# Kernel optimization log

Hardware: AMD Instinct MI355X
Metric: run time of the kernel (lower is better)

The kernel has to match this reference:

```python
import jax, jax.numpy as jnp
import numpy as np

NEG_BIG = -1e10
LEAKY_ALPHA = 0.2

def setup_inputs() -> dict:
    key = jax.random.key(0)
    k1, k2, k3, k4 = jax.random.split(key, 4)
    B, N, F, H = 8, 2048, 128, 4
    X = jax.random.normal(k1, (B, N, F), dtype=jnp.float32)
    A = jax.random.bernoulli(k2, 0.06, (B, N, N)).astype(jnp.float32)
    A = jnp.maximum(A, jnp.eye(N, dtype=jnp.float32)[None])
    attn_self = jax.random.normal(k3, (H, F), dtype=jnp.float32) * 0.1
    attn_neigh = jax.random.normal(k4, (H, F), dtype=jnp.float32) * 0.1
    return {"X": X, "A": A, "attn_self": attn_self, "attn_neigh": attn_neigh}

def reference(X, A, attn_self, attn_neigh):
    # mode 0, concat reduction, tanh activation (applied per head, as in call_mode0)
    B, N, F = X.shape
    H = attn_self.shape[0]
    a_self = jnp.einsum('bnf,hf->bhn', X, attn_self)   # [B,H,N]
    a_neigh = jnp.einsum('bnf,hf->bhn', X, attn_neigh)  # [B,H,N]
    dense = a_self[:, :, :, None] + a_neigh[:, :, None, :]  # [B,H,N,N]
    dense = jnp.where(dense >= 0, dense, LEAKY_ALPHA * dense)  # leaky relu 0.2
    mask = jnp.where(A == 0.0, NEG_BIG, 0.0)[:, None, :, :]   # [B,1,N,N]
    attn = jax.nn.softmax(dense + mask, axis=-1)               # [B,H,N,N]
    feats = jnp.einsum('bhnm,bmf->bhnf', attn, X)              # [B,H,N,F]
    feats = jnp.tanh(feats)
    # concat heads on feature axis -> [B,N,H*F]
    return feats.transpose(0, 2, 1, 3).reshape(B, N, H * F)
```

## Files before the change

### kernel.cpp

```cpp
#include <hip/hip_runtime.h>
#include <hip/hip_bf16.h>
#include <math.h>

#define N_NODES 2048
#define F_DIM   128
#define H_HEADS 4
#define B_BATCH 8
#define LEAKY   0.2f

typedef float f32x4 __attribute__((ext_vector_type(4)));
typedef float f32x2 __attribute__((ext_vector_type(2)));

__device__ __forceinline__ float tanh_fast(float x) {
    const float e = __expf(2.0f * x);
    return 1.0f - 2.0f / (e + 1.0f);
}

__global__ __launch_bounds__(256) void gat_bitpack(const float* __restrict__ A,
                                                   unsigned char* __restrict__ maskb) {
    const int row = blockIdx.x;
    const int tid = threadIdx.x;
    const f32x4* Ar = (const f32x4*)(A + (size_t)row * N_NODES);
    const f32x4 a0 = __builtin_nontemporal_load(Ar + tid * 2);
    const f32x4 a1 = __builtin_nontemporal_load(Ar + tid * 2 + 1);
    unsigned b = 0;
    b |= (a0.x != 0.0f ? 1u : 0u) << 0;
    b |= (a0.y != 0.0f ? 1u : 0u) << 1;
    b |= (a0.z != 0.0f ? 1u : 0u) << 2;
    b |= (a0.w != 0.0f ? 1u : 0u) << 3;
    b |= (a1.x != 0.0f ? 1u : 0u) << 4;
    b |= (a1.y != 0.0f ? 1u : 0u) << 5;
    b |= (a1.z != 0.0f ? 1u : 0u) << 6;
    b |= (a1.w != 0.0f ? 1u : 0u) << 7;
    maskb[(size_t)row * 256 + tid] = (unsigned char)b;
}

__global__ __launch_bounds__(256) void gat_proj(const float* __restrict__ X,
                                                const float* __restrict__ wS,
                                                const float* __restrict__ wN,
                                                float* __restrict__ aSt,
                                                float* __restrict__ aNt) {
    const int wave = threadIdx.x >> 6;
    const int lane = threadIdx.x & 63;
    const int row  = blockIdx.x * 4 + wave;
    const float* xr = X + (size_t)row * F_DIM;
    const float x0 = xr[lane];
    const float x1 = xr[lane + 64];
    float4 ps4, pn4;
    float* psv = (float*)&ps4;
    float* pnv = (float*)&pn4;
#pragma unroll
    for (int h = 0; h < H_HEADS; ++h) {
        float ps = x0 * wS[h * F_DIM + lane] + x1 * wS[h * F_DIM + 64 + lane];
        float pn = x0 * wN[h * F_DIM + lane] + x1 * wN[h * F_DIM + 64 + lane];
#pragma unroll
        for (int off = 32; off > 0; off >>= 1) {
            ps += __shfl_xor(ps, off);
            pn += __shfl_xor(pn, off);
        }
        psv[h] = ps;
        pnv[h] = pn;
    }
    if (lane == 0) {
        ((float4*)aSt)[row] = ps4;
        ((float4*)aNt)[row] = pn4;
    }
}

__global__ __launch_bounds__(256) void gat_gmax(const float* __restrict__ aNt,
                                                float* __restrict__ gmax) {
    const int b = blockIdx.x;
    const int tid = threadIdx.x;
    const int lane = tid & 63;
    const int wv = tid >> 6;
    __shared__ float4 s_part[4];
    float4 m = make_float4(-1e30f, -1e30f, -1e30f, -1e30f);
    const float4* src = (const float4*)aNt + (size_t)b * N_NODES;
    for (int n = tid; n < N_NODES; n += 256) {
        const float4 v = src[n];
        m.x = fmaxf(m.x, v.x); m.y = fmaxf(m.y, v.y);
        m.z = fmaxf(m.z, v.z); m.w = fmaxf(m.w, v.w);
    }
#pragma unroll
    for (int off = 32; off > 0; off >>= 1) {
        m.x = fmaxf(m.x, __shfl_xor(m.x, off));
        m.y = fmaxf(m.y, __shfl_xor(m.y, off));
        m.z = fmaxf(m.z, __shfl_xor(m.z, off));
        m.w = fmaxf(m.w, __shfl_xor(m.w, off));
    }
    if (lane == 0) s_part[wv] = m;
    __syncthreads();
    if (tid == 0) {
        float4 r = s_part[0];
#pragma unroll
        for (int w = 1; w < 4; ++w) {
            r.x = fmaxf(r.x, s_part[w].x); r.y = fmaxf(r.y, s_part[w].y);
            r.z = fmaxf(r.z, s_part[w].z); r.w = fmaxf(r.w, s_part[w].w);
        }
        ((float4*)gmax)[b] = r;
    }
}

#define FMA16(PV, XV)                                        \
    do {                                                     \
        acc[0][0] = fmaf((PV).x, (XV).x, acc[0][0]);         \
        acc[0][1] = fmaf((PV).x, (XV).y, acc[0][1]);         \
        acc[0][2] = fmaf((PV).x, (XV).z, acc[0][2]);         \
        acc[0][3] = fmaf((PV).x, (XV).w, acc[0][3]);         \
        acc[1][0] = fmaf((PV).y, (XV).x, acc[1][0]);         \
        acc[1][1] = fmaf((PV).y, (XV).y, acc[1][1]);         \
        acc[1][2] = fmaf((PV).y, (XV).z, acc[1][2]);         \
        acc[1][3] = fmaf((PV).y, (XV).w, acc[1][3]);         \
        acc[2][0] = fmaf((PV).z, (XV).x, acc[2][0]);         \
        acc[2][1] = fmaf((PV).z, (XV).y, acc[2][1]);         \
        acc[2][2] = fmaf((PV).z, (XV).z, acc[2][2]);         \
        acc[2][3] = fmaf((PV).z, (XV).w, acc[2][3]);         \
        acc[3][0] = fmaf((PV).w, (XV).x, acc[3][0]);         \
        acc[3][1] = fmaf((PV).w, (XV).y, acc[3][1]);         \
        acc[3][2] = fmaf((PV).w, (XV).z, acc[3][2]);         \
        acc[3][3] = fmaf((PV).w, (XV).w, acc[3][3]);         \
    } while (0)

__global__ __launch_bounds__(256, 6) void gat_main(const float* __restrict__ X,
                                                   const unsigned* __restrict__ maskw,
                                                   const float* __restrict__ aSt,
                                                   const float* __restrict__ aNt,
                                                   const float* __restrict__ gmax,
                                                   float* __restrict__ out) {
    const int tid = threadIdx.x;
    const int bid = blockIdx.x;
    const int row = ((bid & 7) << 11) | (bid >> 3);
    const int b = row >> 11;
    const int lane = tid & 63;
    const int wv = tid >> 6;

    __shared__ short  s_idx[N_NODES];
    __shared__ float4 s_p4[256];
    __shared__ int    s_off[256];
    __shared__ float  s_red[4 * 512];
    __shared__ float  s_M[4];
    __shared__ float  s_sv[4];
    __shared__ float  s_scr[16];
    __shared__ int    s_cnt;

    unsigned mw = 0;
    if (tid < 64) mw = maskw[(size_t)row * 64 + tid];

    if (tid >= 64 && tid < 68) {
        const int t = tid - 64;
        const float sv = aSt[(size_t)row * 4 + t];
        const float g = gmax[b * 4 + t];
        float v = sv + g;
        v = fmaxf(v, LEAKY * v);
        s_M[t] = v;
        s_sv[t] = sv;
    }

    if (tid < 64) {
        const int c = __popc(mw);
        int incl = c;
#pragma unroll
        for (int d = 1; d < 64; d <<= 1) {
            const int u = __shfl_up(incl, d);
            if (lane >= d) incl += u;
        }
        if (lane == 63) s_cnt = incl;
        int p = incl - c;
        unsigned m = mw;
        while (m) {
            const int bpos = __ffs(m) - 1;
            s_idx[p++] = (short)((lane << 5) + bpos);
            m &= m - 1;
        }
    }
    __syncthreads();
    const int cnt = s_cnt;

    float acc[4][4];
#pragma unroll
    for (int h = 0; h < 4; ++h)
#pragma unroll
        for (int fi = 0; fi < 4; ++fi) acc[h][fi] = 0.0f;
    float lsum[4] = {0.0f, 0.0f, 0.0f, 0.0f};

    const int jsub = tid >> 5;
    const int f4 = tid & 31;
    const char* XbB = (const char*)(X + (size_t)b * N_NODES * F_DIM) + (f4 << 4);
    const float4* aNb4 = (const float4*)aNt + (size_t)b * N_NODES;

    for (int base = 0; base < cnt; base += 256) {
        const int clen = min(256, cnt - base);
        if (tid < clen) {
            const int m = s_idx[base + tid];
            const float4 t = aNb4[m];
            const float tv[4] = {t.x, t.y, t.z, t.w};
            float4 p4;
            float* pp = (float*)&p4;
#pragma unroll
            for (int h = 0; h < H_HEADS; ++h) {
                float v = s_sv[h] + tv[h];
                v = fmaxf(v, LEAKY * v);
                const float p = __expf(v - s_M[h]);
                pp[h] = p;
                lsum[h] += p;
            }
            s_p4[tid] = p4;
            s_off[tid] = m << 9;
        }
        __syncthreads();
#pragma unroll 4
        for (int j = jsub; j < clen; j += 8) {
            const float4 pv = s_p4[j];
            const float4 xv = *(const float4*)(XbB + (unsigned)s_off[j]);
            FMA16(pv, xv);
        }
        __syncthreads();
    }

#pragma unroll
    for (int h = 0; h < H_HEADS; ++h) {
        float v = lsum[h];
#pragma unroll
        for (int off = 32; off > 0; off >>= 1) v += __shfl_xor(v, off);
        if (lane == 0) s_scr[wv * 4 + h] = v;
    }
#pragma unroll
    for (int h = 0; h < 4; ++h)
#pragma unroll
        for (int fi = 0; fi < 4; ++fi)
            acc[h][fi] += __shfl_xor(acc[h][fi], 32);
    if (lane < 32) {
        float4* red4 = (float4*)s_red;
#pragma unroll
        for (int h = 0; h < 4; ++h)
            red4[wv * 128 + h * 32 + f4] =
                make_float4(acc[h][0], acc[h][1], acc[h][2], acc[h][3]);
    }
    __syncthreads();

    const int hf = tid * 2;
    const int h = tid >> 6;
    const float l = s_scr[h] + s_scr[4 + h] + s_scr[8 + h] + s_scr[12 + h];
    const float invl = 1.0f / l;
    float v0 = 0.0f, v1 = 0.0f;
#pragma unroll
    for (int w = 0; w < 4; ++w) {
        v0 += s_red[w * 512 + hf];
        v1 += s_red[w * 512 + hf + 1];
    }
    f32x2 o;
    o.x = tanh_fast(v0 * invl);
    o.y = tanh_fast(v1 * invl);
    __builtin_nontemporal_store(o, (f32x2*)&out[(size_t)row * 512 + hf]);
}

__global__ __launch_bounds__(256, 6) void gat_main_fb(const float* __restrict__ X,
                                                      const float* __restrict__ A,
                                                      const float* __restrict__ aSt,
                                                      const float* __restrict__ aNt,
                                                      const float* __restrict__ gmax,
                                                      float* __restrict__ out) {
    const int tid = threadIdx.x;
    const int bid = blockIdx.x;
    const int row = ((bid & 7) << 11) | (bid >> 3);
    const int b = row >> 11;
    const int lane = tid & 63;
    const int wv = tid >> 6;

    __shared__ short  s_idx[N_NODES];
    __shared__ float4 s_p4[256];
    __shared__ int    s_off[256];
    __shared__ float  s_red[4 * 512];
    __shared__ int    s_wtot[4];
    __shared__ float  s_M[4];
    __shared__ float  s_sv[4];
    __shared__ float  s_scr[16];

    const f32x4* Arow = (const f32x4*)(A + (size_t)row * N_NODES);
    const f32x4 a0 = __builtin_nontemporal_load(Arow + tid * 2);
    const f32x4 a1 = __builtin_nontemporal_load(Arow + tid * 2 + 1);

    if (tid < 4) {
        const float sv = aSt[(size_t)row * 4 + tid];
        const float g = gmax[b * 4 + tid];
        float v = sv + g;
        v = fmaxf(v, LEAKY * v);
        s_M[tid] = v;
        s_sv[tid] = sv;
    }

    const float av[8] = {a0.x, a0.y, a0.z, a0.w, a1.x, a1.y, a1.z, a1.w};
    int c = 0;
#pragma unroll
    for (int k = 0; k < 8; ++k) c += (av[k] != 0.0f) ? 1 : 0;

    int incl = c;
#pragma unroll
    for (int d = 1; d < 64; d <<= 1) {
        const int u = __shfl_up(incl, d);
        if (lane >= d) incl += u;
    }
    if (lane == 63) s_wtot[wv] = incl;
    __syncthreads();
    int wbase = 0;
#pragma unroll
    for (int w = 0; w < 4; ++w) wbase += (w < wv) ? s_wtot[w] : 0;
    const int cnt = s_wtot[0] + s_wtot[1] + s_wtot[2] + s_wtot[3];
    int pos = wbase + (incl - c);
#pragma unroll
    for (int k = 0; k < 8; ++k) {
        if (av[k] != 0.0f) s_idx[pos++] = (short)(tid * 8 + k);
    }
    __syncthreads();

    float acc[4][4];
#pragma unroll
    for (int h = 0; h < 4; ++h)
#pragma unroll
        for (int fi = 0; fi < 4; ++fi) acc[h][fi] = 0.0f;
    float lsum[4] = {0.0f, 0.0f, 0.0f, 0.0f};

    const int jsub = tid >> 5;
    const int f4 = tid & 31;
    const char* XbB = (const char*)(X + (size_t)b * N_NODES * F_DIM) + (f4 << 4);
    const float4* aNb4 = (const float4*)aNt + (size_t)b * N_NODES;

    for (int base = 0; base < cnt; base += 256) {
        const int clen = min(256, cnt - base);
        if (tid < clen) {
            const int m = s_idx[base + tid];
            const float4 t = aNb4[m];
            const float tv[4] = {t.x, t.y, t.z, t.w};
            float4 p4;
            float* pp = (float*)&p4;
#pragma unroll
            for (int h = 0; h < H_HEADS; ++h) {
                float v = s_sv[h] + tv[h];
                v = fmaxf(v, LEAKY * v);
                const float p = __expf(v - s_M[h]);
                pp[h] = p;
                lsum[h] += p;
            }
            s_p4[tid] = p4;
            s_off[tid] = m << 9;
        }
        __syncthreads();
#pragma unroll 4
        for (int j = jsub; j < clen; j += 8) {
            const float4 pv = s_p4[j];
            const float4 xv = *(const float4*)(XbB + (unsigned)s_off[j]);
            FMA16(pv, xv);
        }
        __syncthreads();
    }

#pragma unroll
    for (int h = 0; h < H_HEADS; ++h) {
        float v = lsum[h];
#pragma unroll
        for (int off = 32; off > 0; off >>= 1) v += __shfl_xor(v, off);
        if (lane == 0) s_scr[wv * 4 + h] = v;
    }
#pragma unroll
    for (int h = 0; h < 4; ++h)
#pragma unroll
        for (int fi = 0; fi < 4; ++fi)
            acc[h][fi] += __shfl_xor(acc[h][fi], 32);
    if (lane < 32) {
        float4* red4 = (float4*)s_red;
#pragma unroll
        for (int h = 0; h < 4; ++h)
            red4[wv * 128 + h * 32 + f4] =
                make_float4(acc[h][0], acc[h][1], acc[h][2], acc[h][3]);
    }
    __syncthreads();

    const int hf = tid * 2;
    const int h = tid >> 6;
    const float l = s_scr[h] + s_scr[4 + h] + s_scr[8 + h] + s_scr[12 + h];
    const float invl = 1.0f / l;
    float v0 = 0.0f, v1 = 0.0f;
#pragma unroll
    for (int w = 0; w < 4; ++w) {
        v0 += s_red[w * 512 + hf];
        v1 += s_red[w * 512 + hf + 1];
    }
    f32x2 o;
    o.x = tanh_fast(v0 * invl);
    o.y = tanh_fast(v1 * invl);
    __builtin_nontemporal_store(o, (f32x2*)&out[(size_t)row * 512 + hf]);
}

extern "C" void kernel_launch(void* const* d_in, const int* in_sizes, int n_in,
                              void* d_out, int out_size, void* d_ws, size_t ws_size,
                              hipStream_t stream) {
    const float* X  = (const float*)d_in[0];
    const float* A  = (const float*)d_in[1];
    const float* wS = (const float*)d_in[2];
    const float* wN = (const float*)d_in[3];
    float* out = (float*)d_out;

    float* aSt = (float*)d_ws;
    float* aNt = aSt + (size_t)B_BATCH * N_NODES * H_HEADS;
    float* gmx = aNt + (size_t)B_BATCH * N_NODES * H_HEADS;
    unsigned char* maskb = (unsigned char*)(gmx + B_BATCH * H_HEADS);

    const size_t need = ((size_t)B_BATCH * N_NODES * H_HEADS * 2 + B_BATCH * H_HEADS) * 4
                        + (size_t)B_BATCH * N_NODES * (N_NODES / 8);

    gat_proj<<<(B_BATCH * N_NODES) / 4, 256, 0, stream>>>(X, wS, wN, aSt, aNt);
    gat_gmax<<<B_BATCH, 256, 0, stream>>>(aNt, gmx);
    if (ws_size >= need) {
        gat_bitpack<<<B_BATCH * N_NODES, 256, 0, stream>>>(A, maskb);
        gat_main<<<B_BATCH * N_NODES, 256, 0, stream>>>(X, (const unsigned*)maskb,
                                                        aSt, aNt, gmx, out);
    } else {
        gat_main_fb<<<B_BATCH * N_NODES, 256, 0, stream>>>(X, A, aSt, aNt, gmx, out);
    }
}
```

Measured before the change: 111.3 us.

## Software-pipeline gathered X loads in GAT aggregation loop with zero-padded chunks

```diff
diff --git a/kernel.cpp b/kernel.cpp
--- a/kernel.cpp
+++ b/kernel.cpp
@@ -21,8 +21,8 @@
     const int row = blockIdx.x;
     const int tid = threadIdx.x;
     const f32x4* Ar = (const f32x4*)(A + (size_t)row * N_NODES);
-    const f32x4 a0 = __builtin_nontemporal_load(Ar + tid * 2);
-    const f32x4 a1 = __builtin_nontemporal_load(Ar + tid * 2 + 1);
+    const f32x4 a0 = Ar[tid * 2];
+    const f32x4 a1 = Ar[tid * 2 + 1];
     unsigned b = 0;
     b |= (a0.x != 0.0f ? 1u : 0u) << 0;
     b |= (a0.y != 0.0f ? 1u : 0u) << 1;
@@ -121,7 +121,7 @@
         acc[3][3] = fmaf((PV).w, (XV).w, acc[3][3]);         \
     } while (0)
 
-__global__ __launch_bounds__(256, 6) void gat_main(const float* __restrict__ X,
+__global__ __launch_bounds__(256, 5) void gat_main(const float* __restrict__ X,
                                                    const unsigned* __restrict__ maskw,
                                                    const float* __restrict__ aSt,
                                                    const float* __restrict__ aNt,
@@ -176,6 +176,9 @@
     __syncthreads();
     const int cnt = s_cnt;
 
+    const float rsv[4] = {s_sv[0], s_sv[1], s_sv[2], s_sv[3]};
+    const float rM[4]  = {s_M[0], s_M[1], s_M[2], s_M[3]};
+
     float acc[4][4];
 #pragma unroll
     for (int h = 0; h < 4; ++h)
@@ -190,6 +193,7 @@
 
     for (int base = 0; base < cnt; base += 256) {
         const int clen = min(256, cnt - base);
+        const int plen = (clen + 31) & ~31;
         if (tid < clen) {
             const int m = s_idx[base + tid];
             const float4 t = aNb4[m];
@@ -198,22 +202,59 @@
             float* pp = (float*)&p4;
 #pragma unroll
             for (int h = 0; h < H_HEADS; ++h) {
-                float v = s_sv[h] + tv[h];
+                float v = rsv[h] + tv[h];
                 v = fmaxf(v, LEAKY * v);
-                const float p = __expf(v - s_M[h]);
+                const float p = __expf(v - rM[h]);
                 pp[h] = p;
                 lsum[h] += p;
             }
             s_p4[tid] = p4;
             s_off[tid] = m << 9;
+        } else {
+            s_p4[tid] = make_float4(0.0f, 0.0f, 0.0f, 0.0f);
+            s_off[tid] = 0;
         }
         __syncthreads();
-#pragma unroll 4
-        for (int j = jsub; j < clen; j += 8) {
-            const float4 pv = s_p4[j];
-            const float4 xv = *(const float4*)(XbB + (unsigned)s_off[j]);
-            FMA16(pv, xv);
-        }
+
+        float4 p0 = s_p4[jsub];
+        float4 p1 = s_p4[jsub + 8];
+        float4 p2 = s_p4[jsub + 16];
+        float4 p3 = s_p4[jsub + 24];
+        const int o0 = s_off[jsub];
+        const int o1 = s_off[jsub + 8];
+        const int o2 = s_off[jsub + 16];
+        const int o3 = s_off[jsub + 24];
+        float4 x0 = *(const float4*)(XbB + (unsigned)o0);
+        float4 x1 = *(const float4*)(XbB + (unsigned)o1);
+        float4 x2 = *(const float4*)(XbB + (unsigned)o2);
+        float4 x3 = *(const float4*)(XbB + (unsigned)o3);
+
+        for (int j = jsub + 32; j < plen; j += 32) {
+            const float4 q0 = s_p4[j];
+            const int    n0 = s_off[j];
+            const float4 q1 = s_p4[j + 8];
+            const int    n1 = s_off[j + 8];
+            const float4 q2 = s_p4[j + 16];
+            const int    n2 = s_off[j + 16];
+            const float4 q3 = s_p4[j + 24];
+            const int    n3 = s_off[j + 24];
+            const float4 y0 = *(const float4*)(XbB + (unsigned)n0);
+            const float4 y1 = *(const float4*)(XbB + (unsigned)n1);
+            const float4 y2 = *(const float4*)(XbB + (unsigned)n2);
+            const float4 y3 = *(const float4*)(XbB + (unsigned)n3);
+            FMA16(p0, x0);
+            p0 = q0; x0 = y0;
+            FMA16(p1, x1);
+            p1 = q1; x1 = y1;
+            FMA16(p2, x2);
+            p2 = q2; x2 = y2;
+            FMA16(p3, x3);
+            p3 = q3; x3 = y3;
+        }
+        FMA16(p0, x0);
+        FMA16(p1, x1);
+        FMA16(p2, x2);
+        FMA16(p3, x3);
         __syncthreads();
     }
 
```

After: 134.5 us. 1.21x slower.

## Stage gathered X rows into LDS via async global_load_lds double buffering

Applied to the files above, without the earlier changes.

```diff
diff --git a/kernel.cpp b/kernel.cpp
--- a/kernel.cpp
+++ b/kernel.cpp
@@ -16,13 +16,19 @@
     return 1.0f - 2.0f / (e + 1.0f);
 }
 
+__device__ __forceinline__ void gload_lds16(const void* g, void* l) {
+    __builtin_amdgcn_global_load_lds(
+        (const __attribute__((address_space(1))) void*)g,
+        (__attribute__((address_space(3))) void*)l, 16, 0, 0);
+}
+
 __global__ __launch_bounds__(256) void gat_bitpack(const float* __restrict__ A,
                                                    unsigned char* __restrict__ maskb) {
     const int row = blockIdx.x;
     const int tid = threadIdx.x;
     const f32x4* Ar = (const f32x4*)(A + (size_t)row * N_NODES);
-    const f32x4 a0 = __builtin_nontemporal_load(Ar + tid * 2);
-    const f32x4 a1 = __builtin_nontemporal_load(Ar + tid * 2 + 1);
+    const f32x4 a0 = Ar[tid * 2];
+    const f32x4 a1 = Ar[tid * 2 + 1];
     unsigned b = 0;
     b |= (a0.x != 0.0f ? 1u : 0u) << 0;
     b |= (a0.y != 0.0f ? 1u : 0u) << 1;
@@ -121,7 +127,7 @@
         acc[3][3] = fmaf((PV).w, (XV).w, acc[3][3]);         \
     } while (0)
 
-__global__ __launch_bounds__(256, 6) void gat_main(const float* __restrict__ X,
+__global__ __launch_bounds__(256, 3) void gat_main(const float* __restrict__ X,
                                                    const unsigned* __restrict__ maskw,
                                                    const float* __restrict__ aSt,
                                                    const float* __restrict__ aNt,
@@ -136,12 +142,12 @@
 
     __shared__ short  s_idx[N_NODES];
     __shared__ float4 s_p4[256];
-    __shared__ int    s_off[256];
-    __shared__ float  s_red[4 * 512];
+    __shared__ float4 s_stage4[2 * 32 * 32];
     __shared__ float  s_M[4];
     __shared__ float  s_sv[4];
     __shared__ float  s_scr[16];
     __shared__ int    s_cnt;
+    float* s_red = (float*)s_stage4;
 
     unsigned mw = 0;
     if (tid < 64) mw = maskw[(size_t)row * 64 + tid];
@@ -176,6 +182,9 @@
     __syncthreads();
     const int cnt = s_cnt;
 
+    const float rsv[4] = {s_sv[0], s_sv[1], s_sv[2], s_sv[3]};
+    const float rM[4]  = {s_M[0], s_M[1], s_M[2], s_M[3]};
+
     float acc[4][4];
 #pragma unroll
     for (int h = 0; h < 4; ++h)
@@ -185,36 +194,70 @@
 
     const int jsub = tid >> 5;
     const int f4 = tid & 31;
-    const char* XbB = (const char*)(X + (size_t)b * N_NODES * F_DIM) + (f4 << 4);
+    const char* XbRow = (const char*)(X + (size_t)b * N_NODES * F_DIM);
     const float4* aNb4 = (const float4*)aNt + (size_t)b * N_NODES;
 
-    for (int base = 0; base < cnt; base += 256) {
-        const int clen = min(256, cnt - base);
-        if (tid < clen) {
-            const int m = s_idx[base + tid];
+    auto ISSUE = [&](int g) {
+        const int so = g << 5;
+        const int l5 = lane >> 5;
+        const int c16 = (lane & 31) << 4;
+        char* lb = ((char*)s_stage4) + ((g & 1) << 14) + (wv << 12);
+#pragma unroll
+        for (int k = 0; k < 4; ++k) {
+            const int q = (wv << 2) + k;
+            const int r = so + (q << 1) + l5;
+            const int m = ((int)s_idx[r & (N_NODES - 1)]) & (N_NODES - 1);
+            const char* gp = XbRow + ((unsigned)m << 9) + c16;
+            gload_lds16(gp, lb + (k << 10));
+        }
+    };
+
+    auto PGEN = [&](int c) {
+        const int gidx = (c << 8) + tid;
+        float4 p4 = make_float4(0.0f, 0.0f, 0.0f, 0.0f);
+        if (gidx < cnt) {
+            const int m = s_idx[gidx];
             const float4 t = aNb4[m];
             const float tv[4] = {t.x, t.y, t.z, t.w};
-            float4 p4;
             float* pp = (float*)&p4;
 #pragma unroll
             for (int h = 0; h < H_HEADS; ++h) {
-                float v = s_sv[h] + tv[h];
+                float v = rsv[h] + tv[h];
                 v = fmaxf(v, LEAKY * v);
-                const float p = __expf(v - s_M[h]);
+                const float p = __expf(v - rM[h]);
                 pp[h] = p;
                 lsum[h] += p;
             }
-            s_p4[tid] = p4;
-            s_off[tid] = m << 9;
-        }
-        __syncthreads();
-#pragma unroll 4
-        for (int j = jsub; j < clen; j += 8) {
-            const float4 pv = s_p4[j];
-            const float4 xv = *(const float4*)(XbB + (unsigned)s_off[j]);
-            FMA16(pv, xv);
-        }
-        __syncthreads();
+        }
+        s_p4[tid] = p4;
+    };
+
+    const int NST = (cnt + 31) >> 5;
+
+    ISSUE(0);
+    PGEN(0);
+
+    for (int gs = 0; gs < NST; ++gs) {
+        const bool more = (gs + 1) < NST;
+        if (gs && ((gs & 7) == 0)) PGEN(gs >> 3);
+        if (more) ISSUE(gs + 1);
+        if (more) { asm volatile("s_waitcnt vmcnt(4) lgkmcnt(0)" ::: "memory"); }
+        else      { asm volatile("s_waitcnt vmcnt(0) lgkmcnt(0)" ::: "memory"); }
+        __builtin_amdgcn_s_barrier();
+        __builtin_amdgcn_sched_barrier(0);
+        {
+            const float* buf = (const float*)s_stage4 + ((gs & 1) * (32 * 128));
+            const int jb = (gs & 7) << 5;
+#pragma unroll
+            for (int k = 0; k < 4; ++k) {
+                const int sr = jsub + (k << 3);
+                const float4 pv = *(const float4*)&s_p4[jb + sr];
+                const float4 xv = *(const float4*)(buf + sr * 128 + (f4 << 2));
+                FMA16(pv, xv);
+            }
+        }
+        __builtin_amdgcn_sched_barrier(0);
+        __builtin_amdgcn_s_barrier();
     }
 
 #pragma unroll
```

New measurement: 171.1 us. 1.54x slower.
